# Kernel optimization log

Measured on AMD Instinct MI355X. Metric: run time of the kernel, lower is better.

Reference implementation:

```python
import jax, jax.numpy as jnp
import numpy as np

EMBED_DIM = 1024
NUM_HEADS = 16
HEAD_DIM = EMBED_DIM // NUM_HEADS


def setup_inputs() -> dict:
    key = jax.random.key(0)
    ks = jax.random.split(key, 5)
    B, S, D = 2, 2048, EMBED_DIM
    bound_qkv = 1.0 / np.sqrt(D)
    bound_out = 1.0 / np.sqrt(D)
    return {
        "x": jax.random.normal(ks[0], (B, S, D), dtype=jnp.float32),
        "w_qkv": jax.random.uniform(ks[1], (3 * D, D), jnp.float32, -bound_qkv, bound_qkv),
        "b_qkv": jax.random.uniform(ks[2], (3 * D,), jnp.float32, -bound_qkv, bound_qkv),
        "w_out": jax.random.uniform(ks[3], (D, D), jnp.float32, -bound_out, bound_out),
        "b_out": jax.random.uniform(ks[4], (D,), jnp.float32, -bound_out, bound_out),
    }


def reference(x, w_qkv, b_qkv, w_out, b_out):
    B, S, D = x.shape
    H, Hd = NUM_HEADS, HEAD_DIM
    qkv = x @ w_qkv.T + b_qkv                      # [B,S,3D]
    q, k, v = jnp.split(qkv, 3, axis=-1)           # each [B,S,D]
    # [B,S,D] -> [B,H,S,Hd]
    q = q.reshape(B, S, H, Hd).transpose(0, 2, 1, 3)
    k = k.reshape(B, S, H, Hd).transpose(0, 2, 1, 3)
    v = v.reshape(B, S, H, Hd).transpose(0, 2, 1, 3)
    scores = jnp.einsum("bhqd,bhkd->bhqk", q, k) / np.sqrt(Hd).astype(np.float32)
    probs = jax.nn.softmax(scores, axis=-1)
    attn = jnp.einsum("bhqk,bhkd->bhqd", probs, v)  # [B,H,S,Hd]
    attn = attn.transpose(0, 2, 1, 3).reshape(B, S, D)
    return attn @ w_out.T + b_out
```

## Files before the change

kernel.cpp:

```cpp
#include <hip/hip_runtime.h>

typedef __bf16 bf16_t;
typedef bf16_t bf16x4 __attribute__((ext_vector_type(4)));
typedef bf16_t bf16x8 __attribute__((ext_vector_type(8)));
typedef float f32x4 __attribute__((ext_vector_type(4)));
typedef float f32x16 __attribute__((ext_vector_type(16)));
typedef unsigned short u16;

#define MFMA16(a, b, c) __builtin_amdgcn_mfma_f32_16x16x32_bf16((a), (b), (c), 0, 0, 0)
#define MFMA32(a, b, c) __builtin_amdgcn_mfma_f32_32x32x16_bf16((a), (b), (c), 0, 0, 0)

#define BATCH 2
#define SEQ   2048
#define DIM   1024
#define NH    16
#define HD    64
#define ROWS  (BATCH * SEQ)
#define QKVN  (3 * DIM)
#define GK    1024

__device__ __forceinline__ u16 f2bf(float f) {
    unsigned u = __float_as_uint(f);
    u += 0x7FFFu + ((u >> 16) & 1u);
    return (u16)(u >> 16);
}

__device__ __forceinline__ float exp2_fast(float x) {
    float r;
    asm("v_exp_f32 %0, %1" : "=v"(r) : "v"(x));
    return r;
}

#define PKBF(lo_, hi_) ({ unsigned r_; \
    asm("v_cvt_pk_bf16_f32 %0, %1, %2" : "=v"(r_) : "v"(lo_), "v"(hi_)); r_; })
#define PLSWAP(a_, b_) \
    asm volatile("v_permlane32_swap_b32 %0, %1" : "+v"(a_), "+v"(b_))

#define GLDS(src, dst) __builtin_amdgcn_global_load_lds( \
    (const __attribute__((address_space(1))) void*)(src), \
    (__attribute__((address_space(3))) void*)(dst), 16, 0, 0)

__global__ __launch_bounds__(256) void cvt_kernel(
    const float* __restrict__ x,  u16* __restrict__ xb,  int nx4,
    const float* __restrict__ w1, u16* __restrict__ w1b, int n14,
    const float* __restrict__ w2, u16* __restrict__ w2b, int n24)
{
    const int total = nx4 + n14 + n24;
    for (int i = blockIdx.x * 256 + threadIdx.x; i < total; i += gridDim.x * 256) {
        const float4* s; ushort4* d; int o;
        if (i < nx4)             { s = (const float4*)x;  d = (ushort4*)xb;  o = i; }
        else if (i < nx4 + n14)  { s = (const float4*)w1; d = (ushort4*)w1b; o = i - nx4; }
        else                     { s = (const float4*)w2; d = (ushort4*)w2b; o = i - nx4 - n14; }
        float4 v = s[o];
        ushort4 r;
        r.x = f2bf(v.x); r.y = f2bf(v.y); r.z = f2bf(v.z); r.w = f2bf(v.w);
        d[o] = r;
    }
}

__global__ __launch_bounds__(512, 2) void gemm_qkv256(
    const u16* __restrict__ A, const u16* __restrict__ Bt,
    const float* __restrict__ bias, u16* __restrict__ C)
{
    __shared__ u16 As[2][256 * 64];
    __shared__ u16 Bs[2][256 * 64];

    const int tid  = threadIdx.x;
    const int lane = tid & 63;
    const int wave = tid >> 6;
    const int r16  = lane & 15;
    const int grp  = lane >> 4;
    const int wm   = wave >> 2, wn = wave & 3;

    int v = (int)blockIdx.x;
    v = (v & 7) * 24 + (v >> 3);
    const int tm = v / 12, tn = v - tm * 12;
    const size_t brow = (size_t)tm * 256;
    const size_t bcol = (size_t)tn * 256;

    const int srow = tid >> 3;
    const int aoff = ((tid & 7) ^ (srow & 7)) * 8;
    const u16* pA = A  + (brow + srow) * (size_t)GK + aoff;
    const u16* pB = Bt + (bcol + srow) * (size_t)GK + aoff;

    f32x4 acc[8][4];
    const f32x4 fz = {0.f, 0.f, 0.f, 0.f};
    #pragma unroll
    for (int m = 0; m < 8; ++m)
        #pragma unroll
        for (int n = 0; n < 4; ++n) acc[m][n] = fz;

    const int sw = r16 & 7;
    #define LDA256(buf, mh, mm, ks) \
        (*(const bf16x8*)&(buf)[(wm*128 + (mh)*64 + (mm)*16 + r16)*64 + ((((ks)*4+grp)^sw)*8)])
    #define LDB256(buf, n, ks) \
        (*(const bf16x8*)&(buf)[(wn*64 + (n)*16 + r16)*64 + ((((ks)*4+grp)^sw)*8)])

    {
        u16* Ad = &As[0][(wave * 8) * 64];
        u16* Bd = &Bs[0][(wave * 8) * 64];
        GLDS(pA, Ad);                 GLDS(pA + 64 * GK,  Ad + 64 * 64);
        GLDS(pA + 128 * GK, Ad + 128 * 64); GLDS(pA + 192 * GK, Ad + 192 * 64);
        GLDS(pB, Bd);                 GLDS(pB + 64 * GK,  Bd + 64 * 64);
        GLDS(pB + 128 * GK, Bd + 128 * 64); GLDS(pB + 192 * GK, Bd + 192 * 64);
    }

    for (int kt = 0; kt < GK / 64; ++kt) {
        const int cur  = kt & 1;
        const bool last = (kt == GK / 64 - 1);
        const int nk = (kt + 1) * 64;
        const u16* Ab = &As[cur][0];
        const u16* Bb = &Bs[cur][0];
        u16* Ad = &As[cur ^ 1][(wave * 8) * 64];
        u16* Bd = &Bs[cur ^ 1][(wave * 8) * 64];
        bf16x8 a[4][2], b0[2][2], b1[2][2];

        if (!last) {
            GLDS(pA + nk, Ad); GLDS(pA + 64 * GK + nk, Ad + 64 * 64);
            asm volatile("s_waitcnt vmcnt(2)" ::: "memory");
        } else {
            asm volatile("s_waitcnt vmcnt(0)" ::: "memory");
        }
        __builtin_amdgcn_s_barrier();
        #pragma unroll
        for (int mm = 0; mm < 4; ++mm) {
            a[mm][0] = LDA256(Ab, 0, mm, 0); a[mm][1] = LDA256(Ab, 0, mm, 1);
        }
        #pragma unroll
        for (int nn = 0; nn < 2; ++nn) {
            b0[nn][0] = LDB256(Bb, nn, 0); b0[nn][1] = LDB256(Bb, nn, 1);
        }
        __builtin_amdgcn_s_setprio(1);
        #pragma unroll
        for (int mm = 0; mm < 4; ++mm)
            #pragma unroll
            for (int nn = 0; nn < 2; ++nn) {
                acc[mm][nn] = MFMA16(a[mm][0], b0[nn][0], acc[mm][nn]);
                acc[mm][nn] = MFMA16(a[mm][1], b0[nn][1], acc[mm][nn]);
            }
        __builtin_amdgcn_s_setprio(0);
        __builtin_amdgcn_s_barrier();

        if (!last) { GLDS(pA + 128 * GK + nk, Ad + 128 * 64);
                     GLDS(pA + 192 * GK + nk, Ad + 192 * 64); }
        #pragma unroll
        for (int nn = 0; nn < 2; ++nn) {
            b1[nn][0] = LDB256(Bb, nn + 2, 0); b1[nn][1] = LDB256(Bb, nn + 2, 1);
        }
        __builtin_amdgcn_s_setprio(1);
        #pragma unroll
        for (int mm = 0; mm < 4; ++mm)
            #pragma unroll
            for (int nn = 0; nn < 2; ++nn) {
                acc[mm][nn + 2] = MFMA16(a[mm][0], b1[nn][0], acc[mm][nn + 2]);
                acc[mm][nn + 2] = MFMA16(a[mm][1], b1[nn][1], acc[mm][nn + 2]);
            }
        __builtin_amdgcn_s_setprio(0);
        __builtin_amdgcn_s_barrier();

        if (!last) { GLDS(pB + nk, Bd); GLDS(pB + 64 * GK + nk, Bd + 64 * 64); }
        #pragma unroll
        for (int mm = 0; mm < 4; ++mm) {
            a[mm][0] = LDA256(Ab, 1, mm, 0); a[mm][1] = LDA256(Ab, 1, mm, 1);
        }
        __builtin_amdgcn_s_setprio(1);
        #pragma unroll
        for (int mm = 0; mm < 4; ++mm)
            #pragma unroll
            for (int nn = 0; nn < 2; ++nn) {
                acc[mm + 4][nn + 2] = MFMA16(a[mm][0], b1[nn][0], acc[mm + 4][nn + 2]);
                acc[mm + 4][nn + 2] = MFMA16(a[mm][1], b1[nn][1], acc[mm + 4][nn + 2]);
            }
        __builtin_amdgcn_s_setprio(0);
        __builtin_amdgcn_s_barrier();

        if (!last) { GLDS(pB + 128 * GK + nk, Bd + 128 * 64);
                     GLDS(pB + 192 * GK + nk, Bd + 192 * 64); }
        __builtin_amdgcn_s_setprio(1);
        #pragma unroll
        for (int mm = 0; mm < 4; ++mm)
            #pragma unroll
            for (int nn = 0; nn < 2; ++nn) {
                acc[mm + 4][nn] = MFMA16(a[mm][0], b0[nn][0], acc[mm + 4][nn]);
                acc[mm + 4][nn] = MFMA16(a[mm][1], b0[nn][1], acc[mm + 4][nn]);
            }
        __builtin_amdgcn_s_setprio(0);
        __builtin_amdgcn_s_barrier();
    }

    #pragma unroll
    for (int n = 0; n < 4; ++n) {
        const size_t col = bcol + wn * 64 + n * 16 + r16;
        const float bv = bias[col];
        #pragma unroll
        for (int m = 0; m < 8; ++m) {
            const size_t row0 = brow + wm * 128 + m * 16 + grp * 4;
            if (tn >= 8) {
                const int c2 = (int)col - 2 * DIM;
                const int d = c2 & 63, h = c2 >> 6;
                const int bb = (int)(row0 >> 11), s0 = (int)(row0 & 2047);
                ushort4 pv;
                pv.x = f2bf(acc[m][n][0] + bv);
                pv.y = f2bf(acc[m][n][1] + bv);
                pv.z = f2bf(acc[m][n][2] + bv);
                pv.w = f2bf(acc[m][n][3] + bv);
                u16* dst = C + ((size_t)bb * 2048 + d * 32 + (s0 >> 6)) * (size_t)QKVN
                             + 2 * DIM + h * 64 + (s0 & 63);
                *(ushort4*)dst = pv;
            } else {
                #pragma unroll
                for (int i = 0; i < 4; ++i)
                    C[(row0 + i) * (size_t)QKVN + col] = f2bf(acc[m][n][i] + bv);
            }
        }
    }
    #undef LDA256
    #undef LDB256
}

__global__ __launch_bounds__(256) void gemm_bt(
    const u16* __restrict__ A, const u16* __restrict__ Bt,
    const float* __restrict__ bias, float* __restrict__ Cv,
    int M, int N, int K)
{
    __shared__ u16 As[128 * 64];
    __shared__ u16 Bs[128 * 64];

    const int tid  = threadIdx.x;
    const int lane = tid & 63;
    const int wave = tid >> 6;
    const int r16  = lane & 15;
    const int grp  = lane >> 4;

    const int nt  = N >> 7;
    const int nwg = (M >> 7) * nt;
    int v = blockIdx.x;
    if ((nwg & 7) == 0) { const int cpx = nwg >> 3; v = (v & 7) * cpx + (v >> 3); }
    const int tm = v / nt, tn = v - tm * nt;
    const size_t brow = (size_t)tm << 7;
    const size_t bcol = (size_t)tn << 7;

    const int wr = wave >> 1, wc = wave & 1;

    f32x4 acc[4][4];
    const f32x4 fz = {0.f, 0.f, 0.f, 0.f};
    #pragma unroll
    for (int m = 0; m < 4; ++m)
        #pragma unroll
        for (int n = 0; n < 4; ++n) acc[m][n] = fz;

    for (int kt = 0; kt < K; kt += 64) {
        #pragma unroll
        for (int it = 0; it < 4; ++it) {
            const int cbase = (it * 4 + wave) * 64;
            const int c   = cbase + lane;
            const int row = c >> 3, cb = c & 7;
            const u16* ga = A  + (brow + row) * (size_t)K + kt + cb * 8;
            const u16* gb = Bt + (bcol + row) * (size_t)K + kt + cb * 8;
            GLDS(ga, &As[cbase * 8]);
            GLDS(gb, &Bs[cbase * 8]);
        }
        __syncthreads();
        #pragma unroll
        for (int ks = 0; ks < 2; ++ks) {
            bf16x8 af[4], bfr[4];
            #pragma unroll
            for (int m = 0; m < 4; ++m)
                af[m] = *(const bf16x8*)&As[(wr * 64 + m * 16 + r16) * 64 + ks * 32 + grp * 8];
            #pragma unroll
            for (int n = 0; n < 4; ++n)
                bfr[n] = *(const bf16x8*)&Bs[(wc * 64 + n * 16 + r16) * 64 + ks * 32 + grp * 8];
            #pragma unroll
            for (int m = 0; m < 4; ++m)
                #pragma unroll
                for (int n = 0; n < 4; ++n)
                    acc[m][n] = MFMA16(af[m], bfr[n], acc[m][n]);
        }
        __syncthreads();
    }

    #pragma unroll
    for (int n = 0; n < 4; ++n) {
        const size_t col = bcol + wc * 64 + n * 16 + r16;
        const float bv = bias[col];
        #pragma unroll
        for (int m = 0; m < 4; ++m) {
            const size_t row0 = brow + wr * 64 + m * 16 + grp * 4;
            #pragma unroll
            for (int i = 0; i < 4; ++i)
                Cv[(row0 + i) * (size_t)N + col] = acc[m][n][i] + bv;
        }
    }
}

__global__ __launch_bounds__(256, 2) void attn_kernel(
    const u16* __restrict__ qkv, u16* __restrict__ attb)
{
    __shared__ u16 kbuf[2][64 * 64];
    __shared__ u16 vbuf[2][64 * 64];

    const int tid  = threadIdx.x;
    const int lane = tid & 63;
    const int wave = tid >> 6;
    const int l31  = lane & 31;
    const int hi   = lane >> 5;
    const int k7   = l31 & 7;

    int v = (int)blockIdx.x;
    v = (v & 7) * 64 + (v >> 3);
    const int bh = v >> 4, qblk = v & 15;
    const int b  = bh >> 4, h = bh & 15;
    const int bS = b * SEQ;
    const int q0w = qblk * 128 + wave * 32;

    bf16x8 qf[4];
    {
        const u16* qp = qkv + (size_t)(bS + q0w + l31) * QKVN + h * HD + hi * 8;
        #pragma unroll
        for (int m = 0; m < 4; ++m) qf[m] = *(const bf16x8*)(qp + m * 16);
    }

    const f32x16 fz16 = {0,0,0,0,0,0,0,0,0,0,0,0,0,0,0,0};
    f32x16 o0 = fz16, o1 = fz16;
    float lsum = 0.f;

    const int r0 = wave * 16 + (lane >> 3);
    const int r1 = r0 + 8;
    const u16* kbase = qkv + (size_t)bS * QKVN + DIM + h * HD;
    const char* kp0 = (const char*)(kbase + (size_t)r0 * QKVN)
                      + (((lane & 7) * 16) ^ ((r0 & 7) << 4));
    const char* kp1 = (const char*)(kbase + (size_t)r1 * QKVN)
                      + (((lane & 7) * 16) ^ ((r1 & 7) << 4));
    const u16* vtb = qkv + (size_t)bS * QKVN + 2 * DIM + h * HD;
    const char* vp0 = (const char*)(vtb + (size_t)(r0 * 32) * QKVN)
                      + (((lane & 7) * 16) ^ ((r0 & 7) << 4));
    const char* vp1 = (const char*)(vtb + (size_t)(r1 * 32) * QKVN)
                      + (((lane & 7) * 16) ^ ((r1 & 7) << 4));

    auto stage = [&](int bsel) {
        u16* kd = &kbuf[bsel][(wave * 16) * 64];
        u16* vd = &vbuf[bsel][(wave * 16) * 64];
        GLDS(kp0, kd);
        GLDS(kp1, kd + 8 * 64);
        GLDS(vp0, vd);
        GLDS(vp1, vd + 8 * 64);
        kp0 += 64 * QKVN * 2; kp1 += 64 * QKVN * 2;
        vp0 += QKVN * 2;      vp1 += QKVN * 2;
    };

    const float C1 = 0.125f * 1.44269504f;
    const float C2 = -8.0f * 1.44269504f;

    auto compute_tile = [&](const u16* kb_, const u16* vb_) {
        const char* kc = (const char*)kb_;
        const char* vc = (const char*)vb_;
        bf16x8 paf[4];

        #pragma unroll
        for (int kt = 0; kt < 2; ++kt) {
            bf16x8 kf[4];
            #pragma unroll
            for (int m = 0; m < 4; ++m)
                kf[m] = *(const bf16x8*)(kc + (kt * 32 + l31) * 128
                                            + (((m * 2 + hi) ^ k7) * 16));
            f32x16 s = fz16;
            __builtin_amdgcn_s_setprio(1);
            #pragma unroll
            for (int m = 0; m < 4; ++m) s = MFMA32(kf[m], qf[m], s);
            __builtin_amdgcn_s_setprio(0);

            float p[16];
            #pragma unroll
            for (int r = 0; r < 16; ++r) {
                p[r] = exp2_fast(fmaf(s[r], C1, C2));
                lsum += p[r];
            }
            unsigned A = PKBF(p[0], p[1]),  Bw = PKBF(p[2], p[3]);
            unsigned C = PKBF(p[4], p[5]),  D  = PKBF(p[6], p[7]);
            unsigned E = PKBF(p[8], p[9]),  F  = PKBF(p[10], p[11]);
            unsigned G = PKBF(p[12], p[13]), H = PKBF(p[14], p[15]);
            PLSWAP(A, C); PLSWAP(Bw, D); PLSWAP(E, G); PLSWAP(F, H);
            union { unsigned u[4]; bf16x8 v8; } w0 = {{A, Bw, C, D}},
                                                w1 = {{E, F, G, H}};
            paf[kt * 2]     = w0.v8;
            paf[kt * 2 + 1] = w1.v8;
        }

        __builtin_amdgcn_s_setprio(1);
        #pragma unroll
        for (int m2 = 0; m2 < 4; ++m2) {
            const int cs = ((m2 * 2 + hi) ^ k7) * 16;
            const bf16x8 vf0 = *(const bf16x8*)(vc + l31 * 128 + cs);
            const bf16x8 vf1 = *(const bf16x8*)(vc + (32 + l31) * 128 + cs);
            o0 = MFMA32(paf[m2], vf0, o0);
            o1 = MFMA32(paf[m2], vf1, o1);
        }
        __builtin_amdgcn_s_setprio(0);
    };

    stage(0);
    asm volatile("s_waitcnt vmcnt(0)" ::: "memory");
    __builtin_amdgcn_s_barrier();

    for (int it = 0; it < SEQ / 128; ++it) {
        stage(1);
        compute_tile(&kbuf[0][0], &vbuf[0][0]);
        asm volatile("s_waitcnt vmcnt(0)" ::: "memory");
        __builtin_amdgcn_s_barrier();
        if (it < SEQ / 128 - 1) stage(0);
        compute_tile(&kbuf[1][0], &vbuf[1][0]);
        asm volatile("s_waitcnt vmcnt(0)" ::: "memory");
        __builtin_amdgcn_s_barrier();
    }

    const float ltot = lsum + __shfl_xor(lsum, 32, 64);
    const float rinv = 1.0f / ltot;

    u16* ob = attb + (size_t)(bS + q0w) * DIM + h * HD + l31;
    #pragma unroll
    for (int r = 0; r < 16; ++r) {
        const int q = (r & 3) + 8 * (r >> 2) + 4 * hi;
        const float iv = __shfl(rinv, q, 64);
        u16* pr = ob + (size_t)q * DIM;
        pr[0]  = f2bf(o0[r] * iv);
        pr[32] = f2bf(o1[r] * iv);
    }
}

extern "C" void kernel_launch(void* const* d_in, const int* in_sizes, int n_in,
                              void* d_out, int out_size, void* d_ws, size_t ws_size,
                              hipStream_t stream)
{
    const float* x     = (const float*)d_in[0];
    const float* w_qkv = (const float*)d_in[1];
    const float* b_qkv = (const float*)d_in[2];
    const float* w_out = (const float*)d_in[3];
    const float* b_out = (const float*)d_in[4];
    float* out = (float*)d_out;

    u16* ws   = (u16*)d_ws;
    u16* XB   = ws;
    u16* WQB  = ws + 4194304;
    u16* WOB  = ws + 7340032;
    u16* QKVB = ws + 8388608;
    u16* ATTB = ws + 20971520;

    cvt_kernel<<<2048, 256, 0, stream>>>(x, XB, (ROWS * DIM) / 4,
                                         w_qkv, WQB, (QKVN * DIM) / 4,
                                         w_out, WOB, (DIM * DIM) / 4);

    gemm_qkv256<<<(ROWS / 256) * (QKVN / 256), 512, 0, stream>>>(
        XB, WQB, b_qkv, QKVB);

    attn_kernel<<<BATCH * NH * (SEQ / 128), 256, 0, stream>>>(QKVB, ATTB);

    gemm_bt<<<(ROWS / 128) * (DIM / 128), 256, 0, stream>>>(
        ATTB, WOB, b_out, out, ROWS, DIM, GK);
}
```

Before: 126.3 us.

## Deepen attention K/V pipeline to four stages and halve out-proj GEMM N tile

The attention kernel moves from double-buffered K/V tiles to a 4-deep ring. It prefetches three tiles ahead and uses partial vmcnt waits instead of draining all loads before every tile, so global-load latency is hidden better. The output-projection GEMM shrinks its N tile from 128 to 64, which doubles the number of workgroups to fill more CUs. That raises A-tile reloads per output, and the larger LDS footprint in attention may lower occupancy.

```diff
diff --git a/kernel.cpp b/kernel.cpp
--- a/kernel.cpp
+++ b/kernel.cpp
@@ -39,6 +39,10 @@
 #define GLDS(src, dst) __builtin_amdgcn_global_load_lds( \
     (const __attribute__((address_space(1))) void*)(src), \
     (__attribute__((address_space(3))) void*)(dst), 16, 0, 0)
+
+#define WAITB(n) do { \
+    asm volatile("s_waitcnt vmcnt(" #n ")" ::: "memory"); \
+    __builtin_amdgcn_s_barrier(); } while (0)
 
 __global__ __launch_bounds__(256) void cvt_kernel(
     const float* __restrict__ x,  u16* __restrict__ xb,  int nx4,
@@ -224,7 +228,7 @@
     int M, int N, int K)
 {
     __shared__ u16 As[128 * 64];
-    __shared__ u16 Bs[128 * 64];
+    __shared__ u16 Bs[64 * 64];
 
     const int tid  = threadIdx.x;
     const int lane = tid & 63;
@@ -232,56 +236,58 @@
     const int r16  = lane & 15;
     const int grp  = lane >> 4;
 
-    const int nt  = N >> 7;
+    const int nt  = N >> 6;
     const int nwg = (M >> 7) * nt;
     int v = blockIdx.x;
     if ((nwg & 7) == 0) { const int cpx = nwg >> 3; v = (v & 7) * cpx + (v >> 3); }
     const int tm = v / nt, tn = v - tm * nt;
     const size_t brow = (size_t)tm << 7;
-    const size_t bcol = (size_t)tn << 7;
+    const size_t bcol = (size_t)tn << 6;
 
     const int wr = wave >> 1, wc = wave & 1;
 
-    f32x4 acc[4][4];
+    f32x4 acc[4][2];
     const f32x4 fz = {0.f, 0.f, 0.f, 0.f};
     #pragma unroll
     for (int m = 0; m < 4; ++m)
         #pragma unroll
-        for (int n = 0; n < 4; ++n) acc[m][n] = fz;
+        for (int n = 0; n < 2; ++n) acc[m][n] = fz;
 
     for (int kt = 0; kt < K; kt += 64) {
         #pragma unroll
         for (int it = 0; it < 4; ++it) {
-            const int cbase = (it * 4 + wave) * 64;
-            const int c   = cbase + lane;
-            const int row = c >> 3, cb = c & 7;
-            const u16* ga = A  + (brow + row) * (size_t)K + kt + cb * 8;
-            const u16* gb = Bt + (bcol + row) * (size_t)K + kt + cb * 8;
-            GLDS(ga, &As[cbase * 8]);
-            GLDS(gb, &Bs[cbase * 8]);
+            const int c = it * 256 + tid;
+            const u16* ga = A + (brow + (c >> 3)) * (size_t)K + kt + (c & 7) * 8;
+            GLDS(ga, &As[(it * 256 + wave * 64) * 8]);
+        }
+        #pragma unroll
+        for (int it = 0; it < 2; ++it) {
+            const int c = it * 256 + tid;
+            const u16* gb = Bt + (bcol + (c >> 3)) * (size_t)K + kt + (c & 7) * 8;
+            GLDS(gb, &Bs[(it * 256 + wave * 64) * 8]);
         }
         __syncthreads();
         #pragma unroll
         for (int ks = 0; ks < 2; ++ks) {
-            bf16x8 af[4], bfr[4];
+            bf16x8 af[4], bfr[2];
             #pragma unroll
             for (int m = 0; m < 4; ++m)
                 af[m] = *(const bf16x8*)&As[(wr * 64 + m * 16 + r16) * 64 + ks * 32 + grp * 8];
             #pragma unroll
-            for (int n = 0; n < 4; ++n)
-                bfr[n] = *(const bf16x8*)&Bs[(wc * 64 + n * 16 + r16) * 64 + ks * 32 + grp * 8];
+            for (int n = 0; n < 2; ++n)
+                bfr[n] = *(const bf16x8*)&Bs[(wc * 32 + n * 16 + r16) * 64 + ks * 32 + grp * 8];
             #pragma unroll
             for (int m = 0; m < 4; ++m)
                 #pragma unroll
-                for (int n = 0; n < 4; ++n)
+                for (int n = 0; n < 2; ++n)
                     acc[m][n] = MFMA16(af[m], bfr[n], acc[m][n]);
         }
         __syncthreads();
     }
 
     #pragma unroll
-    for (int n = 0; n < 4; ++n) {
-        const size_t col = bcol + wc * 64 + n * 16 + r16;
+    for (int n = 0; n < 2; ++n) {
+        const size_t col = bcol + wc * 32 + n * 16 + r16;
         const float bv = bias[col];
         #pragma unroll
         for (int m = 0; m < 4; ++m) {
@@ -296,8 +302,8 @@
 __global__ __launch_bounds__(256, 2) void attn_kernel(
     const u16* __restrict__ qkv, u16* __restrict__ attb)
 {
-    __shared__ u16 kbuf[2][64 * 64];
-    __shared__ u16 vbuf[2][64 * 64];
+    __shared__ u16 kbuf[4][64 * 64];
+    __shared__ u16 vbuf[4][64 * 64];
 
     const int tid  = threadIdx.x;
     const int lane = tid & 63;
@@ -398,20 +404,18 @@
         __builtin_amdgcn_s_setprio(0);
     };
 
-    stage(0);
-    asm volatile("s_waitcnt vmcnt(0)" ::: "memory");
-    __builtin_amdgcn_s_barrier();
-
-    for (int it = 0; it < SEQ / 128; ++it) {
-        stage(1);
-        compute_tile(&kbuf[0][0], &vbuf[0][0]);
-        asm volatile("s_waitcnt vmcnt(0)" ::: "memory");
-        __builtin_amdgcn_s_barrier();
-        if (it < SEQ / 128 - 1) stage(0);
-        compute_tile(&kbuf[1][0], &vbuf[1][0]);
-        asm volatile("s_waitcnt vmcnt(0)" ::: "memory");
-        __builtin_amdgcn_s_barrier();
-    }
+    stage(0); stage(1); stage(2);
+
+    for (int i = 0; i < 7; ++i) {
+        WAITB(8); stage(3); compute_tile(&kbuf[0][0], &vbuf[0][0]);
+        WAITB(8); stage(0); compute_tile(&kbuf[1][0], &vbuf[1][0]);
+        WAITB(8); stage(1); compute_tile(&kbuf[2][0], &vbuf[2][0]);
+        WAITB(8); stage(2); compute_tile(&kbuf[3][0], &vbuf[3][0]);
+    }
+    WAITB(8); stage(3); compute_tile(&kbuf[0][0], &vbuf[0][0]);
+    WAITB(8);           compute_tile(&kbuf[1][0], &vbuf[1][0]);
+    WAITB(4);           compute_tile(&kbuf[2][0], &vbuf[2][0]);
+    WAITB(0);           compute_tile(&kbuf[3][0], &vbuf[3][0]);
 
     const float ltot = lsum + __shfl_xor(lsum, 32, 64);
     const float rinv = 1.0f / ltot;
@@ -454,6 +458,6 @@
 
     attn_kernel<<<BATCH * NH * (SEQ / 128), 256, 0, stream>>>(QKVB, ATTB);
 
-    gemm_bt<<<(ROWS / 128) * (DIM / 128), 256, 0, stream>>>(
+    gemm_bt<<<(ROWS / 128) * (DIM / 64), 256, 0, stream>>>(
         ATTB, WOB, b_out, out, ROWS, DIM, GK);
 }
```

Result: faster. 123.0 us (-2.6%).
